# Optimization experiments

Measured on AMD Instinct MI355X. Metric: run time of the kernel, lower is better.

The kernel has to match this reference:

```python
import jax, jax.numpy as jnp
import numpy as np


def _inside_quad(pts9, quads):
    """Ray-casting point-in-polygon test (semantics of the pointsJf CUDA kernel),
    evaluated only for matched (diagonal) point/box pairs.

    pts9:  [N, 9, 2] points
    quads: [N, 8] polygon corners (x1,y1,x2,y2,x3,y3,x4,y4)
    returns inside flag [N, 9] float32 in {0.0, 1.0}
    """
    vx = quads[:, 0::2][:, None, :]          # [N,1,4]
    vy = quads[:, 1::2][:, None, :]          # [N,1,4]
    vxj = jnp.roll(vx, 1, axis=-1)           # previous vertex (j = i-1 mod 4)
    vyj = jnp.roll(vy, 1, axis=-1)
    px = pts9[..., 0:1]                      # [N,9,1]
    py = pts9[..., 1:2]                      # [N,9,1]
    straddles = (vy > py) != (vyj > py)      # edge crosses horizontal ray
    # x coordinate of edge at height py (only meaningful where straddles)
    x_int = (vxj - vx) * (py - vy) / (vyj - vy) + vx
    crossings = straddles & (px < x_int)     # [N,9,4] bool
    inside = (jnp.sum(crossings.astype(jnp.int32), axis=-1) % 2)
    return inside.astype(jnp.float32)        # [N,9]


def _spatial_border_loss(pts, gt_bboxes, weight, loss_weight):
    n = pts.shape[0]
    pts9 = pts.reshape(n, 9, 2)
    inside = _inside_quad(pts9, gt_bboxes)                    # [N,9]
    out_mask = (inside == 0.0).astype(pts.dtype)              # points outside their gt box
    cx = (gt_bboxes[:, 0] + gt_bboxes[:, 4]) * 0.5
    cy = (gt_bboxes[:, 1] + gt_bboxes[:, 5]) * 0.5
    center = jnp.stack([cx, cy], axis=1)[:, None, :]          # [N,1,2]
    dist = 0.2 * jnp.sqrt(jnp.sum((pts9 - center) ** 2, axis=-1))  # [N,9]
    cnt = jnp.sum(out_mask)
    loss_sb = jnp.where(cnt > 0, jnp.sum(dist * out_mask) / jnp.maximum(cnt, 1.0), 0.0)
    # weighted_spatial_border_loss: avg_factor = sum(weight_repeated4 > 0)/4 + 1e-6
    avg_factor = jnp.sum((weight > 0).astype(jnp.float32)) + 1e-6
    return loss_weight * (loss_sb / avg_factor)[None]          # shape [1]


def setup_inputs() -> dict:
    key = jax.random.key(0)
    k1, k2, k3 = jax.random.split(key, 3)
    N = 1_000_000
    pts = jax.random.normal(k1, (N, 18), dtype=jnp.float32)
    gt_bboxes = jax.random.normal(k2, (N, 8), dtype=jnp.float32)
    weight = jax.random.uniform(k3, (N,), dtype=jnp.float32)
    return {"pts": pts, "gt_bboxes": gt_bboxes, "weight": weight}


def reference(pts, gt_bboxes, weight):
    return _spatial_border_loss(pts, gt_bboxes, weight, loss_weight=1.0)
```

## Files before the change

kernel.cpp:

```cpp
#include <hip/hip_runtime.h>


#define SBL_BLOCK 256
#define SBL_TILE  256

__global__ void __launch_bounds__(SBL_BLOCK) sbl_main(
    const float* __restrict__ pts,
    const float* __restrict__ quads,
    const float* __restrict__ weight,
    double* __restrict__ part_sum,
    unsigned int* __restrict__ part_cnt,
    unsigned int* __restrict__ part_wpos,
    int n)
{
    __shared__ float s_pts[SBL_TILE * 18];

    const int tid  = threadIdx.x;
    const int base = blockIdx.x * SBL_TILE;
    const int rows = min(SBL_TILE, n - base);
    const bool have_row = (tid < rows);

    float local_sum = 0.0f;
    unsigned int local_cnt = 0u, local_wpos = 0u;

    float4 qa = make_float4(0.f, 0.f, 0.f, 0.f);
    float4 qb = make_float4(0.f, 0.f, 0.f, 0.f);
    if (have_row) {
        const float4* q4 = reinterpret_cast<const float4*>(quads) + (size_t)(base + tid) * 2;
        qa = q4[0];
        qb = q4[1];
    }
    {
        const int gi = base + tid;
        if (gi < n) local_wpos = (weight[gi] > 0.0f) ? 1u : 0u;
    }

    if (rows == SBL_TILE) {
        const float4* g4 = reinterpret_cast<const float4*>(pts + (size_t)base * 18);
        float4* s4 = reinterpret_cast<float4*>(s_pts);
        #pragma unroll
        for (int k = 0; k < 5; ++k) {
            const int idx = k * SBL_BLOCK + tid;
            if (idx < (SBL_TILE * 18) / 4) s4[idx] = g4[idx];
        }
    } else {
        const float2* g2 = reinterpret_cast<const float2*>(pts + (size_t)base * 18);
        float2* s2 = reinterpret_cast<float2*>(s_pts);
        const int nf2 = rows * 9;
        for (int idx = tid; idx < nf2; idx += SBL_BLOCK) s2[idx] = g2[idx];
    }
    __syncthreads();

    if (have_row) {
        const float vx0 = qa.x, vy0 = qa.y, vx1 = qa.z, vy1 = qa.w;
        const float vx2 = qb.x, vy2 = qb.y, vx3 = qb.z, vy3 = qb.w;
        const float cx = (vx0 + vx2) * 0.5f;
        const float cy = (vy0 + vy2) * 0.5f;
        const float d0 = vy3 - vy0, d1 = vy0 - vy1, d2 = vy1 - vy2, d3 = vy2 - vy3;
        const float e0 = vx3 - vx0, e1 = vx0 - vx1, e2 = vx1 - vx2, e3 = vx2 - vx3;
        const bool  n0 = d0 < 0.0f, n1 = d1 < 0.0f, n2 = d2 < 0.0f, n3 = d3 < 0.0f;

        const float2* prow = reinterpret_cast<const float2*>(s_pts + tid * 18);
        #pragma unroll
        for (int k = 0; k < 9; ++k) {
            const float2 p = prow[k];
            const float px = p.x, py = p.y;

            const bool c0 = vy0 > py, c1 = vy1 > py, c2 = vy2 > py, c3 = vy3 > py;
            const bool s0 = c0 != c3, s1 = c1 != c0, s2 = c2 != c1, s3 = c3 != c2;

            const float t0 = py - vy0, t1 = py - vy1, t2 = py - vy2, t3 = py - vy3;
            const float m0 = e0 * t0, m1 = e1 * t1, m2 = e2 * t2, m3 = e3 * t3;
            const float l0 = (px - vx0) * d0, l1 = (px - vx1) * d1;
            const float l2 = (px - vx2) * d2, l3 = (px - vx3) * d3;

            const bool x0 = s0 && ((l0 < m0) != n0);
            const bool x1 = s1 && ((l1 < m1) != n1);
            const bool x2 = s2 && ((l2 < m2) != n2);
            const bool x3 = s3 && ((l3 < m3) != n3);

            const bool inside = (x0 != x1) != (x2 != x3);
            if (!inside) {
                const float dx = px - cx;
                const float dy = py - cy;
                local_sum += sqrtf(fmaf(dx, dx, dy * dy));
                local_cnt += 1u;
            }
        }
    }

    #pragma unroll
    for (int off = 32; off > 0; off >>= 1) {
        local_sum  += __shfl_down(local_sum, off, 64);
        local_cnt  += __shfl_down(local_cnt, off, 64);
        local_wpos += __shfl_down(local_wpos, off, 64);
    }

    __shared__ float        r_sum[4];
    __shared__ unsigned int r_cnt[4];
    __shared__ unsigned int r_wpos[4];
    const int lane = tid & 63;
    const int wave = tid >> 6;
    if (lane == 0) { r_sum[wave] = local_sum; r_cnt[wave] = local_cnt; r_wpos[wave] = local_wpos; }
    __syncthreads();
    if (tid == 0) {
        double bsum = 0.0;
        unsigned int bcnt = 0u, bwpos = 0u;
        #pragma unroll
        for (int i = 0; i < 4; ++i) { bsum += (double)r_sum[i]; bcnt += r_cnt[i]; bwpos += r_wpos[i]; }
        part_sum[blockIdx.x]  = bsum;
        part_cnt[blockIdx.x]  = bcnt;
        part_wpos[blockIdx.x] = bwpos;
    }
}

__global__ void __launch_bounds__(256) sbl_finalize(
    const double* __restrict__ part_sum,
    const unsigned int* __restrict__ part_cnt,
    const unsigned int* __restrict__ part_wpos,
    float* __restrict__ out,
    int nblocks)
{
    const int tid = threadIdx.x;
    double s = 0.0;
    unsigned int c = 0u, w = 0u;
    for (int i = tid; i < nblocks; i += 256) {
        s += part_sum[i];
        c += part_cnt[i];
        w += part_wpos[i];
    }
    #pragma unroll
    for (int off = 32; off > 0; off >>= 1) {
        s += __shfl_down(s, off, 64);
        c += __shfl_down(c, off, 64);
        w += __shfl_down(w, off, 64);
    }
    __shared__ double       fs[4];
    __shared__ unsigned int fc[4], fw[4];
    const int lane = tid & 63, wave = tid >> 6;
    if (lane == 0) { fs[wave] = s; fc[wave] = c; fw[wave] = w; }
    __syncthreads();
    if (tid == 0) {
        double ts = 0.0; unsigned int tc = 0u, tw = 0u;
        #pragma unroll
        for (int k = 0; k < 4; ++k) { ts += fs[k]; tc += fc[k]; tw += fw[k]; }
        const double loss_sb = (tc > 0u) ? (0.2 * ts / (double)tc) : 0.0;
        const double avg_factor = (double)tw + 1e-6;
        out[0] = (float)(loss_sb / avg_factor);
    }
}

extern "C" void kernel_launch(void* const* d_in, const int* in_sizes, int n_in,
                              void* d_out, int out_size, void* d_ws, size_t ws_size,
                              hipStream_t stream) {
    const float* pts    = (const float*)d_in[0];
    const float* quads  = (const float*)d_in[1];
    const float* weight = (const float*)d_in[2];
    float* out = (float*)d_out;

    const int n = in_sizes[2];
    const int nblocks = (n + SBL_TILE - 1) / SBL_TILE;

    double*       part_sum  = (double*)d_ws;
    unsigned int* part_cnt  = (unsigned int*)((char*)d_ws + (size_t)nblocks * sizeof(double));
    unsigned int* part_wpos = (unsigned int*)((char*)d_ws + (size_t)nblocks * (sizeof(double) + sizeof(unsigned int)));

    sbl_main<<<nblocks, SBL_BLOCK, 0, stream>>>(pts, quads, weight,
                                                part_sum, part_cnt, part_wpos, n);
    sbl_finalize<<<1, 256, 0, stream>>>(part_sum, part_cnt, part_wpos, out, nblocks);
}
```

Measured before the change: 140.8 us.

## Fuse finalize into main kernel via last-block atomic, enlarge tiles, nontemporal loads

Merges the separate finalize kernel into the main kernel: each block publishes its partials, increments an atomic counter, and the last block to finish performs the final reduction. Block and tile size double to 512 rows, and the global loads switch to nontemporal vector loads. This removes one kernel launch and its dependency gap, at the cost of a memset launch, a threadfence plus atomic per block, and higher LDS use per block (about 36KB), which may lower occupancy.

```diff
diff --git a/kernel.cpp b/kernel.cpp
--- a/kernel.cpp
+++ b/kernel.cpp
@@ -1,55 +1,61 @@
 #include <hip/hip_runtime.h>
 
 
-#define SBL_BLOCK 256
-#define SBL_TILE  256
+typedef float v4f __attribute__((ext_vector_type(4)));
 
-__global__ void __launch_bounds__(SBL_BLOCK) sbl_main(
+#define SBL_BLOCK 512
+#define SBL_TILE  512
+
+__global__ void __launch_bounds__(SBL_BLOCK) sbl_fused(
     const float* __restrict__ pts,
     const float* __restrict__ quads,
     const float* __restrict__ weight,
+    unsigned int* __restrict__ done,
     double* __restrict__ part_sum,
     unsigned int* __restrict__ part_cnt,
     unsigned int* __restrict__ part_wpos,
-    int n)
+    float* __restrict__ out,
+    int n, int nblocks)
 {
     __shared__ float s_pts[SBL_TILE * 18];
+    __shared__ float        r_sum[8];
+    __shared__ unsigned int r_cnt[8];
+    __shared__ unsigned int r_wpos[8];
+    __shared__ unsigned int s_isLast;
+    __shared__ double       f_sum[8];
+    __shared__ unsigned int f_cnt[8];
+    __shared__ unsigned int f_wpos[8];
 
     const int tid  = threadIdx.x;
     const int base = blockIdx.x * SBL_TILE;
-    const int rows = min(SBL_TILE, n - base);
+    int rows = n - base; if (rows > SBL_TILE) rows = SBL_TILE;
     const bool have_row = (tid < rows);
 
-    float local_sum = 0.0f;
-    unsigned int local_cnt = 0u, local_wpos = 0u;
-
-    float4 qa = make_float4(0.f, 0.f, 0.f, 0.f);
-    float4 qb = make_float4(0.f, 0.f, 0.f, 0.f);
+    v4f qa = {0.f, 0.f, 0.f, 0.f};
+    v4f qb = {0.f, 0.f, 0.f, 0.f};
+    float wv = 0.0f;
     if (have_row) {
-        const float4* q4 = reinterpret_cast<const float4*>(quads) + (size_t)(base + tid) * 2;
-        qa = q4[0];
-        qb = q4[1];
-    }
-    {
-        const int gi = base + tid;
-        if (gi < n) local_wpos = (weight[gi] > 0.0f) ? 1u : 0u;
+        const v4f* q4 = reinterpret_cast<const v4f*>(quads) + (size_t)(base + tid) * 2;
+        qa = __builtin_nontemporal_load(q4);
+        qb = __builtin_nontemporal_load(q4 + 1);
+        wv = __builtin_nontemporal_load(&weight[base + tid]);
     }
 
-    if (rows == SBL_TILE) {
-        const float4* g4 = reinterpret_cast<const float4*>(pts + (size_t)base * 18);
-        float4* s4 = reinterpret_cast<float4*>(s_pts);
-        #pragma unroll
-        for (int k = 0; k < 5; ++k) {
-            const int idx = k * SBL_BLOCK + tid;
-            if (idx < (SBL_TILE * 18) / 4) s4[idx] = g4[idx];
-        }
-    } else {
-        const float2* g2 = reinterpret_cast<const float2*>(pts + (size_t)base * 18);
-        float2* s2 = reinterpret_cast<float2*>(s_pts);
-        const int nf2 = rows * 9;
-        for (int idx = tid; idx < nf2; idx += SBL_BLOCK) s2[idx] = g2[idx];
+    {
+        const v4f* g4 = reinterpret_cast<const v4f*>(pts + (size_t)base * 18);
+        v4f* s4 = reinterpret_cast<v4f*>(s_pts);
+        const int nfloats = rows * 18;
+        const int nf4 = nfloats >> 2;
+        for (int idx = tid; idx < nf4; idx += SBL_BLOCK)
+            s4[idx] = __builtin_nontemporal_load(&g4[idx]);
+        for (int idx = (nf4 << 2) + tid; idx < nfloats; idx += SBL_BLOCK)
+            s_pts[idx] = pts[(size_t)base * 18 + idx];
     }
     __syncthreads();
+
+    float local_sum = 0.0f;
+    unsigned int local_cnt = 0u;
+    unsigned int local_wpos = (wv > 0.0f) ? 1u : 0u;
 
     if (have_row) {
         const float vx0 = qa.x, vy0 = qa.y, vx1 = qa.z, vy1 = qa.w;
@@ -96,9 +102,6 @@
         local_wpos += __shfl_down(local_wpos, off, 64);
     }
 
-    __shared__ float        r_sum[4];
-    __shared__ unsigned int r_cnt[4];
-    __shared__ unsigned int r_wpos[4];
     const int lane = tid & 63;
     const int wave = tid >> 6;
     if (lane == 0) { r_sum[wave] = local_sum; r_cnt[wave] = local_cnt; r_wpos[wave] = local_wpos; }
@@ -107,46 +110,41 @@
         double bsum = 0.0;
         unsigned int bcnt = 0u, bwpos = 0u;
         #pragma unroll
-        for (int i = 0; i < 4; ++i) { bsum += (double)r_sum[i]; bcnt += r_cnt[i]; bwpos += r_wpos[i]; }
+        for (int i = 0; i < 8; ++i) { bsum += (double)r_sum[i]; bcnt += r_cnt[i]; bwpos += r_wpos[i]; }
         part_sum[blockIdx.x]  = bsum;
         part_cnt[blockIdx.x]  = bcnt;
         part_wpos[blockIdx.x] = bwpos;
+        __threadfence();
+        unsigned int prev = atomicAdd(done, 1u);
+        s_isLast = (prev == (unsigned int)(nblocks - 1)) ? 1u : 0u;
     }
-}
+    __syncthreads();
 
-__global__ void __launch_bounds__(256) sbl_finalize(
-    const double* __restrict__ part_sum,
-    const unsigned int* __restrict__ part_cnt,
-    const unsigned int* __restrict__ part_wpos,
-    float* __restrict__ out,
-    int nblocks)
-{
-    const int tid = threadIdx.x;
-    double s = 0.0;
-    unsigned int c = 0u, w = 0u;
-    for (int i = tid; i < nblocks; i += 256) {
-        s += part_sum[i];
-        c += part_cnt[i];
-        w += part_wpos[i];
-    }
-    #pragma unroll
-    for (int off = 32; off > 0; off >>= 1) {
-        s += __shfl_down(s, off, 64);
-        c += __shfl_down(c, off, 64);
-        w += __shfl_down(w, off, 64);
-    }
-    __shared__ double       fs[4];
-    __shared__ unsigned int fc[4], fw[4];
-    const int lane = tid & 63, wave = tid >> 6;
-    if (lane == 0) { fs[wave] = s; fc[wave] = c; fw[wave] = w; }
-    __syncthreads();
-    if (tid == 0) {
-        double ts = 0.0; unsigned int tc = 0u, tw = 0u;
+    if (s_isLast) {
+        __threadfence();
+        double s = 0.0;
+        unsigned int c = 0u, w = 0u;
+        for (int i = tid; i < nblocks; i += SBL_BLOCK) {
+            s += part_sum[i];
+            c += part_cnt[i];
+            w += part_wpos[i];
+        }
         #pragma unroll
-        for (int k = 0; k < 4; ++k) { ts += fs[k]; tc += fc[k]; tw += fw[k]; }
-        const double loss_sb = (tc > 0u) ? (0.2 * ts / (double)tc) : 0.0;
-        const double avg_factor = (double)tw + 1e-6;
-        out[0] = (float)(loss_sb / avg_factor);
+        for (int off = 32; off > 0; off >>= 1) {
+            s += __shfl_down(s, off, 64);
+            c += __shfl_down(c, off, 64);
+            w += __shfl_down(w, off, 64);
+        }
+        if (lane == 0) { f_sum[wave] = s; f_cnt[wave] = c; f_wpos[wave] = w; }
+        __syncthreads();
+        if (tid == 0) {
+            double ts = 0.0; unsigned int tc = 0u, tw = 0u;
+            #pragma unroll
+            for (int i = 0; i < 8; ++i) { ts += f_sum[i]; tc += f_cnt[i]; tw += f_wpos[i]; }
+            const double loss_sb = (tc > 0u) ? (0.2 * ts / (double)tc) : 0.0;
+            const double avg_factor = (double)tw + 1e-6;
+            out[0] = (float)(loss_sb / avg_factor);
+        }
     }
 }
 
@@ -161,11 +159,13 @@
     const int n = in_sizes[2];
     const int nblocks = (n + SBL_TILE - 1) / SBL_TILE;
 
-    double*       part_sum  = (double*)d_ws;
-    unsigned int* part_cnt  = (unsigned int*)((char*)d_ws + (size_t)nblocks * sizeof(double));
-    unsigned int* part_wpos = (unsigned int*)((char*)d_ws + (size_t)nblocks * (sizeof(double) + sizeof(unsigned int)));
+    unsigned int* done      = (unsigned int*)d_ws;
+    double*       part_sum  = (double*)((char*)d_ws + 16);
+    unsigned int* part_cnt  = (unsigned int*)((char*)d_ws + 16 + (size_t)nblocks * 8);
+    unsigned int* part_wpos = (unsigned int*)((char*)d_ws + 16 + (size_t)nblocks * 12);
 
-    sbl_main<<<nblocks, SBL_BLOCK, 0, stream>>>(pts, quads, weight,
-                                                part_sum, part_cnt, part_wpos, n);
-    sbl_finalize<<<1, 256, 0, stream>>>(part_sum, part_cnt, part_wpos, out, nblocks);
+    hipMemsetAsync(done, 0, sizeof(unsigned int), stream);
+    sbl_fused<<<nblocks, SBL_BLOCK, 0, stream>>>(pts, quads, weight,
+                                                 done, part_sum, part_cnt, part_wpos,
+                                                 out, n, nblocks);
 }
```

Measured after the change: 174.6 us. +24.0%, slower.
